# Performance work log

Hardware: AMD Instinct MI355X
Metric: run time of the kernel (lower is better)

## Reference

```python
import jax, jax.numpy as jnp
import numpy as np

N_DETS = 8192
DEG = 64
E = N_DETS * DEG
NUM_BLOCKS = 8
SHORTCUT = 128   # shortcutDim
RED = 32         # reducedDim
INNER = 64       # blockInnerDim = 2*32
PW_RAW = 9
PW_HID = 256
PW_OUT = 32


def setup_inputs() -> dict:
    key = jax.random.key(0)
    ks = jax.random.split(key, 24)
    # valid boxes: x2 > x1, y2 > y1
    x1 = jax.random.uniform(ks[0], (N_DETS, 1), jnp.float32, 0.0, 1000.0)
    y1 = jax.random.uniform(ks[1], (N_DETS, 1), jnp.float32, 0.0, 1000.0)
    w = jax.random.uniform(ks[2], (N_DETS, 1), jnp.float32, 8.0, 128.0)
    h = jax.random.uniform(ks[3], (N_DETS, 1), jnp.float32, 8.0, 128.0)
    dtBoxes = jnp.concatenate([x1, y1, x1 + w, y1 + h], axis=1)
    detScores = jax.random.uniform(ks[4], (N_DETS, 1), jnp.float32)
    # every detection has DEG neighbors (first one is itself) -> no empty segments
    cIdxs = jnp.repeat(jnp.arange(N_DETS, dtype=jnp.int32), DEG)
    nIdxs = jax.random.randint(ks[5], (E,), 0, N_DETS, dtype=jnp.int32)
    nIdxs = nIdxs.at[::DEG].set(jnp.arange(N_DETS, dtype=jnp.int32))
    detFeatures = jnp.zeros((N_DETS, SHORTCUT), jnp.float32)

    def lin(k, fan_in, fan_out):
        b = 1.0 / np.sqrt(fan_in)
        return jax.random.uniform(k, (fan_in, fan_out), jnp.float32, -b, b)

    inp = dict(detScores=detScores, dtBoxes=dtBoxes, detFeatures=detFeatures,
               cIdxs=cIdxs, nIdxs=nIdxs)
    # pairwise feature generator MLP: 9 -> 256 -> 256 -> 32 (ReLU after each)
    inp['pw_W0'] = lin(ks[6], PW_RAW, PW_HID); inp['pw_b0'] = jnp.zeros((PW_HID,), jnp.float32)
    inp['pw_W1'] = lin(ks[7], PW_HID, PW_HID); inp['pw_b1'] = jnp.zeros((PW_HID,), jnp.float32)
    inp['pw_W2'] = lin(ks[8], PW_HID, PW_OUT); inp['pw_b2'] = jnp.zeros((PW_OUT,), jnp.float32)
    # per-block params, stacked over NUM_BLOCKS
    B = NUM_BLOCKS
    inp['blk_fc1_W'] = jnp.stack([lin(jax.random.fold_in(ks[9], i), SHORTCUT, RED) for i in range(B)])
    inp['blk_fc1_b'] = jnp.zeros((B, RED), jnp.float32)
    inp['blk_pw1_W'] = jnp.stack([lin(jax.random.fold_in(ks[10], i), 3 * RED, INNER) for i in range(B)])
    inp['blk_pw1_b'] = jnp.zeros((B, INNER), jnp.float32)
    inp['blk_pw2_W'] = jnp.stack([lin(jax.random.fold_in(ks[11], i), INNER, INNER) for i in range(B)])
    inp['blk_pw2_b'] = jnp.zeros((B, INNER), jnp.float32)
    inp['blk_post_W'] = jnp.stack([jnp.stack([lin(jax.random.fold_in(ks[12], 2 * i + j), INNER, INNER) for j in range(2)]) for i in range(B)])
    inp['blk_post_b'] = jnp.zeros((B, 2, INNER), jnp.float32)
    inp['blk_out_W'] = jnp.stack([lin(jax.random.fold_in(ks[13], i), INNER, SHORTCUT) for i in range(B)])
    inp['blk_out_b'] = jnp.zeros((B, SHORTCUT), jnp.float32)
    return inp


def _pairwise_raw(detScores, dtBoxes, cIdxs, nIdxs):
    # box data (getBoxData)
    x1, y1, x2, y2 = (dtBoxes[:, i:i + 1] for i in range(4))
    w, h = x2 - x1, y2 - y1
    area = w * h
    c, n = cIdxs, nIdxs
    # per-edge IoU (dt_dt_iou gathered at (c,n))
    ix = jnp.maximum(0.0, jnp.minimum(x2[c], x2[n]) - jnp.maximum(x1[c], x1[n]))
    iy = jnp.maximum(0.0, jnp.minimum(y2[c], y2[n]) - jnp.maximum(y1[c], y1[n]))
    inter = ix * iy
    iou = inter / (area[c] + area[n] - inter)
    c_w, c_h, n_w, n_h = w[c], h[c], w[n], h[n]
    c_scale = (c_w + c_h) / 2.0
    c_cx, c_cy = x1[c] + c_w / 2.0, y1[c] + c_h / 2.0
    n_cx, n_cy = x1[n] + n_w / 2.0, y1[n] + n_h / 2.0
    x_dist = n_cx - c_cx
    y_dist = n_cy - c_cy
    l2_dist = jnp.sqrt(x_dist ** 2 + y_dist ** 2) / c_scale
    x_dist = x_dist / c_scale
    y_dist = y_dist / c_scale
    log2 = jnp.log(jnp.float32(2.0))
    w_diff = jnp.log(n_w / c_w) / log2
    h_diff = jnp.log(n_h / c_h) / log2
    aspect_diff = (jnp.log(n_w / n_h) - jnp.log(c_w / c_h)) / log2
    return jnp.concatenate([detScores[c], detScores[n], iou, x_dist, y_dist,
                            l2_dist, w_diff, h_diff, aspect_diff], axis=1)  # [E,9]


def reference(detScores, dtBoxes, detFeatures, pw_W0, pw_b0, pw_W1, pw_b1,
              pw_W2, pw_b2, blk_fc1_W, blk_fc1_b, blk_pw1_W, blk_pw1_b,
              blk_pw2_W, blk_pw2_b, blk_post_W, blk_post_b, blk_out_W,
              blk_out_b, cIdxs, nIdxs):
    relu = jax.nn.relu
    numDets = detFeatures.shape[0]
    raw = _pairwise_raw(detScores, dtBoxes, cIdxs, nIdxs)
    pf = relu(raw @ pw_W0 + pw_b0)
    pf = relu(pf @ pw_W1 + pw_b1)
    pairFeatures = relu(pf @ pw_W2 + pw_b2)  # [E,32]

    f = detFeatures
    for i in range(blk_fc1_W.shape[0]):
        f1 = relu(f @ blk_fc1_W[i] + blk_fc1_b[i])                       # [N,32]
        comb = jnp.concatenate([pairFeatures, f1[cIdxs], f1[nIdxs]], 1)  # [E,96]
        comb = relu(comb @ blk_pw1_W[i] + blk_pw1_b[i])
        comb = relu(comb @ blk_pw2_W[i] + blk_pw2_b[i])                  # [E,64]
        pooled = jax.ops.segment_max(comb, cIdxs, num_segments=numDets)  # [N,64]
        pooled = relu(pooled @ blk_post_W[i, 0] + blk_post_b[i, 0])
        pooled = relu(pooled @ blk_post_W[i, 1] + blk_post_b[i, 1])
        f = relu(f + pooled @ blk_out_W[i] + blk_out_b[i])               # [N,128]
    return f
```

## Files before the change

kernel.cpp:

```cpp
#include <hip/hip_runtime.h>
#include <hip/hip_bf16.h>

typedef _Float16 half8 __attribute__((ext_vector_type(8)));
typedef __fp16 fp16x2 __attribute__((ext_vector_type(2)));
typedef float f32x4 __attribute__((ext_vector_type(4)));

#define N_DETS 8192

#define OFF_W0P   0
#define OFF_W1P   8192
#define OFF_W2P   73728
#define OFF_FC1P  81920
#define OFF_PW1P  114688
#define OFF_PW2P  163840
#define OFF_POSTP 196608
#define OFF_OUTP  262144
#define OFF_F1A   327680
#define OFF_F1B   589824
#define OFF_PFP   1114112
#define OFF_FBUF_BYTES 35782656


__device__ inline f32x4 mfma16(half8 a, half8 b, f32x4 c){
  return __builtin_amdgcn_mfma_f32_16x16x32_f16(a, b, c, 0, 0, 0);
}
__device__ inline half8 ldg8(const _Float16* p){ return *(const half8*)p; }

__device__ inline unsigned pkrtz(float a, float b){
  union { fp16x2 h; unsigned u; } x;
  x.h = __builtin_amdgcn_cvt_pkrtz(a, b);
  return x.u;
}
__device__ inline unsigned hmax2u(unsigned a, unsigned b){
  unsigned r;
  asm("v_pk_max_f16 %0, %1, %2" : "=v"(r) : "v"(a), "v"(b));
  return r;
}
__device__ inline unsigned hadd2u(unsigned a, unsigned b){
  unsigned r;
  asm("v_pk_add_f16 %0, %1, %2" : "=v"(r) : "v"(a), "v"(b));
  return r;
}

__device__ inline half8 cvtpack(f32x4 A, f32x4 B){
  union { unsigned w[4]; half8 h; } r;
  r.w[0] = pkrtz(A[0], A[1]); r.w[1] = pkrtz(A[2], A[3]);
  r.w[2] = pkrtz(B[0], B[1]); r.w[3] = pkrtz(B[2], B[3]);
  return r.h;
}
__device__ inline half8 cvtpackbr(f32x4 A, f32x4 B, const unsigned* pb){
  union { unsigned w[4]; half8 h; } r;
  r.w[0] = pkrtz(A[0], A[1]); r.w[1] = pkrtz(A[2], A[3]);
  r.w[2] = pkrtz(B[0], B[1]); r.w[3] = pkrtz(B[2], B[3]);
#pragma unroll
  for (int i = 0; i < 4; ++i) r.w[i] = hmax2u(hadd2u(r.w[i], pb[i]), 0u);
  return r.h;
}
__device__ inline half8 cvtpackr(f32x4 A, f32x4 B){
  union { unsigned w[4]; half8 h; } r;
  r.w[0] = pkrtz(A[0], A[1]); r.w[1] = pkrtz(A[2], A[3]);
  r.w[2] = pkrtz(B[0], B[1]); r.w[3] = pkrtz(B[2], B[3]);
#pragma unroll
  for (int i = 0; i < 4; ++i) r.w[i] = hmax2u(r.w[i], 0u);
  return r.h;
}

__device__ inline void packB(const float* W, int Ksrc, int Nn, _Float16* dst, int sig){
  int ns = (Ksrc + 31) >> 5;
  int t = sig / (ns * 64);
  int rem = sig - t * ns * 64;
  int s = rem >> 6;
  int l = rem & 63;
  int col = t * 16 + (l & 15);
  int g = l >> 4;
  half8 v;
#pragma unroll
  for (int j = 0; j < 8; ++j){
    int k = s*32 + ((j>>2)<<4) + g*4 + (j&3);
    v[j] = (_Float16)((k < Ksrc) ? W[k * Nn + col] : 0.f);
  }
  *(half8*)(dst + sig * 8) = v;
}

__device__ inline void packW0(const float* W, const float* bias, _Float16* dst, int sig){
  int t = sig >> 6, l = sig & 63;
  int col = t * 16 + (l & 15);
  int g = l >> 4;
  half8 v;
#pragma unroll
  for (int j = 0; j < 8; ++j){
    int k = ((j>>2)<<4) + g*4 + (j&3);
    float x = 0.f;
    if (k < 9) x = W[k * 256 + col];
    else if (k == 9) x = bias[col];
    v[j] = (_Float16)x;
  }
  *(half8*)(dst + sig * 8) = v;
}

__global__ __launch_bounds__(256) void kPrep(const float* pwW0, const float* pwb0,
    const float* pwW1, const float* pwW2,
    const float* fc1W, const float* pw1W, const float* pw2W, const float* postW, const float* outW,
    _Float16* wsh){
  int sig = blockIdx.x * 256 + threadIdx.x;
  if (sig < 1024){ packW0(pwW0, pwb0, wsh + OFF_W0P, sig); return; }
  sig -= 1024;
  if (sig < 8192){ packB(pwW1, 256, 256, wsh + OFF_W1P, sig); return; }
  sig -= 8192;
  if (sig < 1024){ packB(pwW2, 256, 32, wsh + OFF_W2P, sig); return; }
  sig -= 1024;
  int i = sig / 3840;
  int q = sig - i * 3840;
  if (q < 512){ packB(fc1W + i*4096, 128, 32, wsh + OFF_FC1P + i*4096, q); return; }
  q -= 512;
  if (q < 768){ packB(pw1W + i*6144, 96, 64, wsh + OFF_PW1P + i*6144, q); return; }
  q -= 768;
  if (q < 512){ packB(pw2W + i*4096, 64, 64, wsh + OFF_PW2P + i*4096, q); return; }
  q -= 512;
  if (q < 512){ packB(postW + i*8192, 64, 64, wsh + OFF_POSTP + i*8192, q); return; }
  q -= 512;
  if (q < 512){ packB(postW + i*8192 + 4096, 64, 64, wsh + OFF_POSTP + i*8192 + 4096, q); return; }
  q -= 512;
  packB(outW + i*8192, 64, 128, wsh + OFF_OUTP + i*8192, q);
}

__global__ __launch_bounds__(256, 2) void kP(const float* scores, const float* boxes,
    const int* cI, const int* nI, const float* b1, const float* b2,
    const _Float16* W0p, const _Float16* W1p, const _Float16* W2p, _Float16* pfp){
  __shared__ __align__(16) _Float16 sbuf[2][8192];
  int tid = threadIdx.x;
  int lane = tid & 63, wave = tid >> 6;
  const f32x4 fz = {0.f, 0.f, 0.f, 0.f};

  half8 w0ld[4], s0ld[4];
#pragma unroll
  for (int it = 0; it < 4; ++it){
    w0ld[it] = ldg8(W0p + it*2048 + tid*8);
    s0ld[it] = ldg8(W1p + it*2048 + tid*8);
  }
  {
    half8 z = {0,0,0,0,0,0,0,0};
#pragma unroll
    for (int it = 0; it < 4; ++it) *(half8*)(&sbuf[1][0] + it*2048 + tid*8) = z;
  }
#pragma unroll
  for (int it = 0; it < 4; ++it)
    *(half8*)(&sbuf[0][0] + it*2048 + tid*8) = w0ld[it];
  __syncthreads();
  {
    int e = blockIdx.x*256 + tid;
    int c = cI[e], n = nI[e];
    float cx1 = boxes[c*4+0], cy1 = boxes[c*4+1], cx2 = boxes[c*4+2], cy2 = boxes[c*4+3];
    float nx1 = boxes[n*4+0], ny1 = boxes[n*4+1], nx2 = boxes[n*4+2], ny2 = boxes[n*4+3];
    float cw = cx2-cx1, ch = cy2-cy1, nw = nx2-nx1, nh = ny2-ny1;
    float ca = cw*ch, na = nw*nh;
    float ix = fmaxf(fminf(cx2,nx2) - fmaxf(cx1,nx1), 0.f);
    float iy = fmaxf(fminf(cy2,ny2) - fmaxf(cy1,ny1), 0.f);
    float inter = ix*iy;
    float iou = inter / (ca + na - inter);
    float cs = (cw + ch) * 0.5f;
    float xd = (nx1 + nw*0.5f) - (cx1 + cw*0.5f);
    float yd = (ny1 + nh*0.5f) - (cy1 + ch*0.5f);
    float l2 = sqrtf(xd*xd + yd*yd) / cs;
    float wd = log2f(nw/cw), hd = log2f(nh/ch);
    float ad = log2f(nw/nh) - log2f(cw/ch);
    float rv[10] = {scores[c], scores[n], iou, xd/cs, yd/cs, l2, wd, hd, ad, 1.0f};
    int base = (tid >> 4) * 512;
    int r = tid & 15;
#pragma unroll
    for (int k = 0; k < 10; ++k)
      sbuf[1][base + (((k>>2)&3)*16 + r)*8 + (k&3)] = (_Float16)rv[k];
  }
  __syncthreads();

  half8 h0f[4][8];
  {
    half8 braw[4];
#pragma unroll
    for (int et = 0; et < 4; ++et)
      braw[et] = *(const half8*)(&sbuf[1][0] + ((wave*4+et)*64 + lane)*8);
#pragma unroll
    for (int mp = 0; mp < 8; ++mp){
      half8 A0 = *(const half8*)(&sbuf[0][0] + (2*mp)*512   + lane*8);
      half8 A1 = *(const half8*)(&sbuf[0][0] + (2*mp+1)*512 + lane*8);
#pragma unroll
      for (int et = 0; et < 4; ++et){
        f32x4 a = mfma16(A0, braw[et], fz);
        f32x4 b = mfma16(A1, braw[et], fz);
        h0f[et][mp] = cvtpackr(a, b);
      }
    }
  }
  __syncthreads();
#pragma unroll
  for (int it = 0; it < 4; ++it)
    *(half8*)(&sbuf[1][0] + it*2048 + tid*8) = s0ld[it];
  __syncthreads();

  int q = lane >> 4;
  f32x4 apf[4][2];
#pragma unroll
  for (int et = 0; et < 4; ++et){ apf[et][0] = fz; apf[et][1] = fz; }
  for (int mp = 0; mp < 8; ++mp){
    const _Float16* cur = &sbuf[(mp+1)&1][0];
    half8 stg[4];
    if (mp < 7){
#pragma unroll
      for (int it = 0; it < 4; ++it)
        stg[it] = ldg8(W1p + (mp+1)*8192 + it*2048 + tid*8);
    }
    f32x4 acc[4][2];
#pragma unroll
    for (int et = 0; et < 4; ++et){ acc[et][0] = fz; acc[et][1] = fz; }
#pragma unroll
    for (int s = 0; s < 8; ++s){
      half8 A0 = *(const half8*)(cur + s*512       + lane*8);
      half8 A1 = *(const half8*)(cur + (8+s)*512   + lane*8);
#pragma unroll
      for (int et = 0; et < 4; ++et){
        acc[et][0] = mfma16(A0, h0f[et][s], acc[et][0]);
        acc[et][1] = mfma16(A1, h0f[et][s], acc[et][1]);
      }
    }
    unsigned pb[4];
    pb[0] = pkrtz(b1[mp*32 + q*4 + 0], b1[mp*32 + q*4 + 1]);
    pb[1] = pkrtz(b1[mp*32 + q*4 + 2], b1[mp*32 + q*4 + 3]);
    pb[2] = pkrtz(b1[mp*32 + 16 + q*4 + 0], b1[mp*32 + 16 + q*4 + 1]);
    pb[3] = pkrtz(b1[mp*32 + 16 + q*4 + 2], b1[mp*32 + 16 + q*4 + 3]);
    half8 w2a = ldg8(W2p + mp*512 + lane*8);
    half8 w2b = ldg8(W2p + (8+mp)*512 + lane*8);
#pragma unroll
    for (int et = 0; et < 4; ++et){
      half8 h1f = cvtpackbr(acc[et][0], acc[et][1], pb);
      apf[et][0] = mfma16(w2a, h1f, apf[et][0]);
      apf[et][1] = mfma16(w2b, h1f, apf[et][1]);
    }
    if (mp < 7){
      _Float16* nxt = &sbuf[mp&1][0];
#pragma unroll
      for (int it = 0; it < 4; ++it)
        *(half8*)(nxt + it*2048 + tid*8) = stg[it];
    }
    __syncthreads();
  }
  unsigned pc[4];
  pc[0] = pkrtz(b2[q*4 + 0], b2[q*4 + 1]);
  pc[1] = pkrtz(b2[q*4 + 2], b2[q*4 + 3]);
  pc[2] = pkrtz(b2[16 + q*4 + 0], b2[16 + q*4 + 1]);
  pc[3] = pkrtz(b2[16 + q*4 + 2], b2[16 + q*4 + 3]);
#pragma unroll
  for (int et = 0; et < 4; ++et){
    half8 pf = cvtpackbr(apf[et][0], apf[et][1], pc);
    *(half8*)(pfp + (blockIdx.x*16 + wave*4 + et)*512 + lane*8) = pf;
  }
}

__global__ __launch_bounds__(256) void kF1(const float* detF, const _Float16* fc1p,
    const float* fb, _Float16* f1G){
  int lane = threadIdx.x & 63, wave = threadIdx.x >> 6;
  int q = lane >> 4, e = lane & 15;
  int det = (blockIdx.x * 4 + wave) * 16 + e;
  const f32x4 fz = {0.f, 0.f, 0.f, 0.f};
  half8 ff[4];
#pragma unroll
  for (int s = 0; s < 4; ++s){
    const float* p = detF + det*128 + s*32 + q*4;
    f32x4 x0 = *(const f32x4*)(p);
    f32x4 x1 = *(const f32x4*)(p + 16);
    union { unsigned w[4]; half8 h; } u;
    u.w[0] = pkrtz(x0[0], x0[1]); u.w[1] = pkrtz(x0[2], x0[3]);
    u.w[2] = pkrtz(x1[0], x1[1]); u.w[3] = pkrtz(x1[2], x1[3]);
    ff[s] = u.h;
  }
#pragma unroll
  for (int m = 0; m < 2; ++m){
    f32x4 a = fz;
#pragma unroll
    for (int s = 0; s < 4; ++s)
      a = mfma16(ldg8(fc1p + (m*4+s)*512 + lane*8), ff[s], a);
    f32x4 bv = *(const f32x4*)(fb + m*16 + q*4);
    unsigned u0 = pkrtz(fmaxf(a[0]+bv[0],0.f), fmaxf(a[1]+bv[1],0.f));
    unsigned u1 = pkrtz(fmaxf(a[2]+bv[2],0.f), fmaxf(a[3]+bv[3],0.f));
    *(unsigned*)(f1G + det*32 + q*8 + m*4)     = u0;
    *(unsigned*)(f1G + det*32 + q*8 + m*4 + 2) = u1;
  }
}

__global__ __launch_bounds__(256) void kBlk(const _Float16* pfp, const _Float16* f1in,
    _Float16* f1out, const int* nI, const _Float16* pw1p, const _Float16* pw2p,
    const _Float16* post0p, const _Float16* post1p, const _Float16* outp, const _Float16* fc1pn,
    const float* bb1, const float* bb2, const float* pb0, const float* pb1, const float* ob,
    const float* fbn, const float* fin, float* fout, int doF1){
  __shared__ __align__(16) _Float16 poolS[1024];
  __shared__ __align__(16) _Float16 ffS[2048];
  int tid = threadIdx.x, lane = tid & 63, wave = tid >> 6;
  int q = lane >> 4, e = lane & 15;
  int bid = blockIdx.x;
  int base = ((bid & 7) * 64 + (bid >> 3)) * 16;
  const f32x4 fz = {0.f, 0.f, 0.f, 0.f};

  half8 aW1[4][3], aW2[4][2];
  f32x4 b1v[4];
  unsigned b2p[8];
#pragma unroll
  for (int m = 0; m < 4; ++m){
#pragma unroll
    for (int k = 0; k < 3; ++k) aW1[m][k] = ldg8(pw1p + (m*3+k)*512 + lane*8);
#pragma unroll
    for (int k = 0; k < 2; ++k) aW2[m][k] = ldg8(pw2p + (m*2+k)*512 + lane*8);
    b1v[m] = *(const f32x4*)(bb1 + m*16 + q*4);
    b2p[m*2+0] = pkrtz(bb2[m*16 + q*4 + 0], bb2[m*16 + q*4 + 1]);
    b2p[m*2+1] = pkrtz(bb2[m*16 + q*4 + 2], bb2[m*16 + q*4 + 3]);
  }

  int nnC[4]; half8 BcC;
  {
    int det0 = base + wave*4;
#pragma unroll
    for (int et = 0; et < 4; ++et) nnC[et] = nI[det0*64 + et*16 + e];
    BcC = ldg8(f1in + det0*32 + q*8);
  }
#pragma unroll 1
  for (int dd = 0; dd < 4; ++dd){
    int d = wave*4 + dd;
    int det = base + d;
    half8 Bpf[4], Bn[4];
#pragma unroll
    for (int et = 0; et < 4; ++et){
      Bpf[et] = ldg8(pfp + (det*4+et)*512 + lane*8);
      Bn[et]  = ldg8(f1in + nnC[et]*32 + q*8);
    }
    int nnN[4]; half8 BcN;
    if (dd < 3){
      int detn = det + 1;
#pragma unroll
      for (int et = 0; et < 4; ++et) nnN[et] = nI[detn*64 + et*16 + e];
      BcN = ldg8(f1in + detn*32 + q*8);
    }
    f32x4 bcb[4];
#pragma unroll
    for (int m = 0; m < 4; ++m){
      f32x4 dc = mfma16(aW1[m][1], BcC, fz);
#pragma unroll
      for (int r = 0; r < 4; ++r) bcb[m][r] = dc[r] + b1v[m][r];
    }
    unsigned pm[8];
#pragma unroll
    for (int i = 0; i < 8; ++i) pm[i] = 0xFC00FC00u;
#pragma unroll
    for (int et = 0; et < 4; ++et){
      f32x4 acc[4];
#pragma unroll
      for (int m = 0; m < 4; ++m){
        acc[m] = mfma16(aW1[m][0], Bpf[et], fz);
        acc[m] = mfma16(aW1[m][2], Bn[et], acc[m]);
      }
      f32x4 r0, r1, r2, r3;
#pragma unroll
      for (int r = 0; r < 4; ++r){
        r0[r] = fmaxf(acc[0][r] + bcb[0][r], 0.f);
        r1[r] = fmaxf(acc[1][r] + bcb[1][r], 0.f);
        r2[r] = fmaxf(acc[2][r] + bcb[2][r], 0.f);
        r3[r] = fmaxf(acc[3][r] + bcb[3][r], 0.f);
      }
      half8 h1a = cvtpack(r0, r1);
      half8 h1b = cvtpack(r2, r3);
      f32x4 a2[4];
#pragma unroll
      for (int m = 0; m < 4; ++m){
        a2[m] = mfma16(aW2[m][0], h1a, fz);
        a2[m] = mfma16(aW2[m][1], h1b, a2[m]);
      }
      union { half8 h; unsigned w[4]; } uA, uB;
      uA.h = cvtpack(a2[0], a2[1]);
      uB.h = cvtpack(a2[2], a2[3]);
#pragma unroll
      for (int i = 0; i < 4; ++i){
        pm[i]   = hmax2u(pm[i],   uA.w[i]);
        pm[4+i] = hmax2u(pm[4+i], uB.w[i]);
      }
    }
#pragma unroll
    for (int s = 1; s <= 8; s <<= 1){
#pragma unroll
      for (int i = 0; i < 8; ++i)
        pm[i] = hmax2u(pm[i], __shfl_xor(pm[i], s));
    }
#pragma unroll
    for (int i = 0; i < 8; ++i)
      pm[i] = hmax2u(hadd2u(pm[i], b2p[i]), 0u);
    if (e == 0){
      union { unsigned w[4]; half8 h; } o0, o1;
#pragma unroll
      for (int i = 0; i < 4; ++i){ o0.w[i] = pm[i]; o1.w[i] = pm[4+i]; }
      *(half8*)(poolS + d*32 + q*8)       = o0.h;
      *(half8*)(poolS + 512 + d*32 + q*8) = o1.h;
    }
    if (dd < 3){
#pragma unroll
      for (int et = 0; et < 4; ++et) nnC[et] = nnN[et];
      BcC = BcN;
    }
  }
  __syncthreads();

  half8 Bp0 = *(const half8*)(poolS + e*32 + q*8);
  half8 Bp1 = *(const half8*)(poolS + 512 + e*32 + q*8);
  int det = base + e;
  f32x4 t0[4];
#pragma unroll
  for (int m = 0; m < 4; ++m){
    f32x4 a = mfma16(ldg8(post0p + (m*2)*512   + lane*8), Bp0, fz);
    a = mfma16(ldg8(post0p + (m*2+1)*512 + lane*8), Bp1, a);
    f32x4 bv = *(const f32x4*)(pb0 + m*16 + q*4);
#pragma unroll
    for (int r = 0; r < 4; ++r) t0[m][r] = fmaxf(a[r] + bv[r], 0.f);
  }
  half8 p1a = cvtpack(t0[0], t0[1]);
  half8 p1b = cvtpack(t0[2], t0[3]);
#pragma unroll
  for (int m = 0; m < 4; ++m){
    f32x4 a = mfma16(ldg8(post1p + (m*2)*512   + lane*8), p1a, fz);
    a = mfma16(ldg8(post1p + (m*2+1)*512 + lane*8), p1b, a);
    f32x4 bv = *(const f32x4*)(pb1 + m*16 + q*4);
#pragma unroll
    for (int r = 0; r < 4; ++r) t0[m][r] = fmaxf(a[r] + bv[r], 0.f);
  }
  half8 p2a = cvtpack(t0[0], t0[1]);
  half8 p2b = cvtpack(t0[2], t0[3]);
  int m0 = wave*2, m1 = m0 + 1;
  f32x4 fr0, fr1;
  {
    f32x4 a = mfma16(ldg8(outp + (m0*2)*512   + lane*8), p2a, fz);
    a = mfma16(ldg8(outp + (m0*2+1)*512 + lane*8), p2b, a);
    f32x4 bv = *(const f32x4*)(ob + m0*16 + q*4);
    f32x4 fv = *(const f32x4*)(fin + det*128 + m0*16 + q*4);
#pragma unroll
    for (int r = 0; r < 4; ++r) fr0[r] = fmaxf(fv[r] + a[r] + bv[r], 0.f);
  }
  {
    f32x4 a = mfma16(ldg8(outp + (m1*2)*512   + lane*8), p2a, fz);
    a = mfma16(ldg8(outp + (m1*2+1)*512 + lane*8), p2b, a);
    f32x4 bv = *(const f32x4*)(ob + m1*16 + q*4);
    f32x4 fv = *(const f32x4*)(fin + det*128 + m1*16 + q*4);
#pragma unroll
    for (int r = 0; r < 4; ++r) fr1[r] = fmaxf(fv[r] + a[r] + bv[r], 0.f);
  }
  *(f32x4*)(fout + det*128 + m0*16 + q*4) = fr0;
  *(f32x4*)(fout + det*128 + m1*16 + q*4) = fr1;
  if (doF1){
    half8 ffw = cvtpack(fr0, fr1);
    *(half8*)(ffS + wave*512 + lane*8) = ffw;
    __syncthreads();
    if (wave == 0){
#pragma unroll
      for (int m = 0; m < 2; ++m){
        f32x4 a = fz;
#pragma unroll
        for (int s = 0; s < 4; ++s){
          half8 fs = *(const half8*)(ffS + s*512 + lane*8);
          a = mfma16(ldg8(fc1pn + (m*4+s)*512 + lane*8), fs, a);
        }
        f32x4 bv = *(const f32x4*)(fbn + m*16 + q*4);
        unsigned u0 = pkrtz(fmaxf(a[0]+bv[0],0.f), fmaxf(a[1]+bv[1],0.f));
        unsigned u1 = pkrtz(fmaxf(a[2]+bv[2],0.f), fmaxf(a[3]+bv[3],0.f));
        *(unsigned*)(f1out + det*32 + q*8 + m*4)     = u0;
        *(unsigned*)(f1out + det*32 + q*8 + m*4 + 2) = u1;
      }
    }
  }
}

extern "C" void kernel_launch(void* const* d_in, const int* in_sizes, int n_in,
                              void* d_out, int out_size, void* d_ws, size_t ws_size,
                              hipStream_t stream){
  const float* detScores   = (const float*)d_in[0];
  const float* dtBoxes     = (const float*)d_in[1];
  const float* detFeatures = (const float*)d_in[2];
  const int*   cI          = (const int*)d_in[3];
  const int*   nI          = (const int*)d_in[4];
  const float* pwW0 = (const float*)d_in[5];
  const float* pwb0 = (const float*)d_in[6];
  const float* pwW1 = (const float*)d_in[7];
  const float* pwb1 = (const float*)d_in[8];
  const float* pwW2 = (const float*)d_in[9];
  const float* pwb2 = (const float*)d_in[10];
  const float* fc1W = (const float*)d_in[11];
  const float* fc1b = (const float*)d_in[12];
  const float* pw1W = (const float*)d_in[13];
  const float* pw1b = (const float*)d_in[14];
  const float* pw2W = (const float*)d_in[15];
  const float* pw2b = (const float*)d_in[16];
  const float* postW = (const float*)d_in[17];
  const float* postb = (const float*)d_in[18];
  const float* outW  = (const float*)d_in[19];
  const float* outb  = (const float*)d_in[20];

  _Float16* wsh  = (_Float16*)d_ws;
  float*    fbuf = (float*)((char*)d_ws + OFF_FBUF_BYTES);
  _Float16* f1A  = wsh + OFF_F1A;
  _Float16* f1B  = wsh + OFF_F1B;
  _Float16* pfp  = wsh + OFF_PFP;

  kPrep<<<160, 256, 0, stream>>>(pwW0, pwb0, pwW1, pwW2, fc1W, pw1W, pw2W, postW, outW, wsh);
  kF1<<<128, 256, 0, stream>>>(detFeatures, wsh + OFF_FC1P, fc1b, f1A);
  kP<<<2048, 256, 0, stream>>>(detScores, dtBoxes, cI, nI, pwb1, pwb2,
      wsh + OFF_W0P, wsh + OFF_W1P, wsh + OFF_W2P, pfp);

  for (int i = 0; i < 8; ++i){
    int last = (i == 7);
    _Float16* fin1  = (i & 1) ? f1B : f1A;
    _Float16* fout1 = (i & 1) ? f1A : f1B;
    kBlk<<<512, 256, 0, stream>>>(pfp, fin1, fout1, nI,
        wsh + OFF_PW1P + i*6144, wsh + OFF_PW2P + i*4096,
        wsh + OFF_POSTP + i*8192, wsh + OFF_POSTP + i*8192 + 4096, wsh + OFF_OUTP + i*8192,
        wsh + OFF_FC1P + ((i+1) & 7)*4096,
        pw1b + i*64, pw2b + i*64, postb + i*128, postb + i*128 + 64, outb + i*128,
        fc1b + ((i+1) & 7)*32,
        (i == 0) ? detFeatures : fbuf, last ? (float*)d_out : fbuf, last ? 0 : 1);
  }
}
```

Baseline: 236.4 us.

## Fuse eight block-layer launches into one cooperative kernel with grid sync

Replaces the eight per-layer kBlk launches with a single persistent cooperative kernel that loops over layers and separates them with grid.sync(). The aim is to remove per-launch overhead and the gaps between dependent kernels. If the cooperative launch fails, it falls back to the original launches. Grid-wide barriers cost something themselves, and all 512 blocks of 256 threads must fit on the device at once for the cooperative launch to succeed.

```diff
diff --git a/kernel.cpp b/kernel.cpp
--- a/kernel.cpp
+++ b/kernel.cpp
@@ -1,5 +1,8 @@
 #include <hip/hip_runtime.h>
 #include <hip/hip_bf16.h>
+#include <hip/hip_cooperative_groups.h>
+
+namespace cg = cooperative_groups;
 
 typedef _Float16 half8 __attribute__((ext_vector_type(8)));
 typedef __fp16 fp16x2 __attribute__((ext_vector_type(2)));
@@ -19,7 +22,6 @@
 #define OFF_F1B   589824
 #define OFF_PFP   1114112
 #define OFF_FBUF_BYTES 35782656
-
 
 __device__ inline f32x4 mfma16(half8 a, half8 b, f32x4 c){
   return __builtin_amdgcn_mfma_f32_16x16x32_f16(a, b, c, 0, 0, 0);
@@ -286,17 +288,14 @@
   }
 }
 
-__global__ __launch_bounds__(256) void kBlk(const _Float16* pfp, const _Float16* f1in,
+__device__ inline void blkBody(const _Float16* pfp, const _Float16* f1in,
     _Float16* f1out, const int* nI, const _Float16* pw1p, const _Float16* pw2p,
     const _Float16* post0p, const _Float16* post1p, const _Float16* outp, const _Float16* fc1pn,
     const float* bb1, const float* bb2, const float* pb0, const float* pb1, const float* ob,
-    const float* fbn, const float* fin, float* fout, int doF1){
-  __shared__ __align__(16) _Float16 poolS[1024];
-  __shared__ __align__(16) _Float16 ffS[2048];
-  int tid = threadIdx.x, lane = tid & 63, wave = tid >> 6;
+    const float* fbn, const float* fin, float* fout, int doF1,
+    _Float16* poolS, _Float16* ffS, int base, int tid){
+  int lane = tid & 63, wave = tid >> 6;
   int q = lane >> 4, e = lane & 15;
-  int bid = blockIdx.x;
-  int base = ((bid & 7) * 64 + (bid >> 3)) * 16;
   const f32x4 fz = {0.f, 0.f, 0.f, 0.f};
 
   half8 aW1[4][3], aW2[4][2];
@@ -468,6 +467,46 @@
         *(unsigned*)(f1out + det*32 + q*8 + m*4 + 2) = u1;
       }
     }
+  }
+}
+
+__global__ __launch_bounds__(256) void kBlk(const _Float16* pfp, const _Float16* f1in,
+    _Float16* f1out, const int* nI, const _Float16* pw1p, const _Float16* pw2p,
+    const _Float16* post0p, const _Float16* post1p, const _Float16* outp, const _Float16* fc1pn,
+    const float* bb1, const float* bb2, const float* pb0, const float* pb1, const float* ob,
+    const float* fbn, const float* fin, float* fout, int doF1){
+  __shared__ __align__(16) _Float16 poolS[1024];
+  __shared__ __align__(16) _Float16 ffS[2048];
+  int bid = blockIdx.x;
+  int base = ((bid & 7) * 64 + (bid >> 3)) * 16;
+  blkBody(pfp, f1in, f1out, nI, pw1p, pw2p, post0p, post1p, outp, fc1pn,
+          bb1, bb2, pb0, pb1, ob, fbn, fin, fout, doF1,
+          poolS, ffS, base, threadIdx.x);
+}
+
+__global__ __launch_bounds__(256) void kBlkAll(const _Float16* pfp, _Float16* f1Ap,
+    _Float16* f1Bp, const int* nI, const _Float16* wsh,
+    const float* pw1b, const float* pw2b, const float* postb, const float* outb,
+    const float* fc1b, const float* detF, float* fbuf, float* dout){
+  __shared__ __align__(16) _Float16 poolS[1024];
+  __shared__ __align__(16) _Float16 ffS[2048];
+  cg::grid_group grid = cg::this_grid();
+  int bid = blockIdx.x;
+  int base = ((bid & 7) * 64 + (bid >> 3)) * 16;
+  for (int i = 0; i < 8; ++i){
+    int last = (i == 7);
+    blkBody(pfp,
+            (i & 1) ? f1Bp : f1Ap,
+            (i & 1) ? f1Ap : f1Bp,
+            nI,
+            wsh + OFF_PW1P + i*6144, wsh + OFF_PW2P + i*4096,
+            wsh + OFF_POSTP + i*8192, wsh + OFF_POSTP + i*8192 + 4096,
+            wsh + OFF_OUTP + i*8192, wsh + OFF_FC1P + ((i+1)&7)*4096,
+            pw1b + i*64, pw2b + i*64, postb + i*128, postb + i*128 + 64,
+            outb + i*128, fc1b + ((i+1)&7)*32,
+            (i == 0) ? detF : fbuf, last ? dout : fbuf, last ? 0 : 1,
+            poolS, ffS, base, threadIdx.x);
+    if (!last) grid.sync();
   }
 }
 
@@ -507,16 +546,28 @@
   kP<<<2048, 256, 0, stream>>>(detScores, dtBoxes, cI, nI, pwb1, pwb2,
       wsh + OFF_W0P, wsh + OFF_W1P, wsh + OFF_W2P, pfp);
 
-  for (int i = 0; i < 8; ++i){
-    int last = (i == 7);
-    _Float16* fin1  = (i & 1) ? f1B : f1A;
-    _Float16* fout1 = (i & 1) ? f1A : f1B;
-    kBlk<<<512, 256, 0, stream>>>(pfp, fin1, fout1, nI,
-        wsh + OFF_PW1P + i*6144, wsh + OFF_PW2P + i*4096,
-        wsh + OFF_POSTP + i*8192, wsh + OFF_POSTP + i*8192 + 4096, wsh + OFF_OUTP + i*8192,
-        wsh + OFF_FC1P + ((i+1) & 7)*4096,
-        pw1b + i*64, pw2b + i*64, postb + i*128, postb + i*128 + 64, outb + i*128,
-        fc1b + ((i+1) & 7)*32,
-        (i == 0) ? detFeatures : fbuf, last ? (float*)d_out : fbuf, last ? 0 : 1);
-  }
-}
+  const _Float16* pfp_c = pfp;
+  const _Float16* wsh_c = wsh;
+  float* dout = (float*)d_out;
+  void* kargs[] = {
+    (void*)&pfp_c, (void*)&f1A, (void*)&f1B, (void*)&nI, (void*)&wsh_c,
+    (void*)&pw1b, (void*)&pw2b, (void*)&postb, (void*)&outb, (void*)&fc1b,
+    (void*)&detFeatures, (void*)&fbuf, (void*)&dout
+  };
+  hipError_t rc = hipLaunchCooperativeKernel((const void*)kBlkAll, dim3(512), dim3(256),
+                                             kargs, 0, stream);
+  if (rc != hipSuccess){
+    for (int i = 0; i < 8; ++i){
+      int last = (i == 7);
+      _Float16* fin1  = (i & 1) ? f1B : f1A;
+      _Float16* fout1 = (i & 1) ? f1A : f1B;
+      kBlk<<<512, 256, 0, stream>>>(pfp, fin1, fout1, nI,
+          wsh + OFF_PW1P + i*6144, wsh + OFF_PW2P + i*4096,
+          wsh + OFF_POSTP + i*8192, wsh + OFF_POSTP + i*8192 + 4096, wsh + OFF_OUTP + i*8192,
+          wsh + OFF_FC1P + ((i+1) & 7)*4096,
+          pw1b + i*64, pw2b + i*64, postb + i*128, postb + i*128 + 64, outb + i*128,
+          fc1b + ((i+1) & 7)*32,
+          (i == 0) ? detFeatures : fbuf, last ? (float*)d_out : fbuf, last ? 0 : 1);
+    }
+  }
+}
```

Measured after the change: 631.7 us. +167.2%, slower.
